# Optimization experiments

Hardware: AMD Instinct MI355X
Metric: run time of the kernel (lower is better)

The kernel has to match this reference:

```python
import jax, jax.numpy as jnp
import numpy as np
import math

HEAD = 4
HEAD_DIM = 16
K_ATT = 7
PAD_ATT = 3  # (dilation*(kernel_att-1)+1)//2 with dilation=1, kernel_att=7
K_CONV = 3


def closest_factor_to_sqrt(n):
    if n <= 1:
        return n
    sqrt_n = int(math.sqrt(n))
    if sqrt_n * sqrt_n == n:
        return sqrt_n
    best, best_diff = 1, float('inf')
    for i in range(sqrt_n, 0, -1):
        if n % i == 0:
            diff = abs(i - n // i)
            if diff < best_diff:
                best_diff, best = diff, i
    return best


def setup_inputs() -> dict:
    key = jax.random.key(0)
    ks = jax.random.split(key, 10)
    Cin, Cout = 64, 64
    x = jax.random.normal(ks[0], (2, Cin, 8, 32, 32), dtype=jnp.float32)
    w1 = jax.random.normal(ks[1], (Cout, Cin), dtype=jnp.float32) * 0.05
    b1 = jax.random.normal(ks[2], (Cout,), dtype=jnp.float32) * 0.01
    w2 = jax.random.normal(ks[3], (Cout, Cin), dtype=jnp.float32) * 0.05
    b2 = jax.random.normal(ks[4], (Cout,), dtype=jnp.float32) * 0.01
    w3 = jax.random.normal(ks[5], (Cout, Cin), dtype=jnp.float32) * 0.05
    b3 = jax.random.normal(ks[6], (Cout,), dtype=jnp.float32) * 0.01
    wp = jax.random.normal(ks[7], (HEAD_DIM, 3), dtype=jnp.float32) * 0.05
    bp = jnp.zeros((HEAD_DIM,), dtype=jnp.float32)
    wfc = jax.random.normal(ks[8], (K_CONV * K_CONV, 3 * HEAD), dtype=jnp.float32) * 0.05
    # dep_conv init per reset_parameters(): identity shift kernels, zero bias
    ident = jnp.eye(K_CONV * K_CONV, dtype=jnp.float32).reshape(K_CONV * K_CONV, K_CONV, K_CONV)
    wdep = jnp.tile(ident[None], (Cout, 1, 1, 1))  # (Cout, 9, 3, 3), groups=head_dim
    bdep = jnp.zeros((Cout,), dtype=jnp.float32)
    rate1 = jnp.array(0.5, dtype=jnp.float32)
    rate2 = jnp.array(0.5, dtype=jnp.float32)
    return {'x': x, 'w1': w1, 'b1': b1, 'w2': w2, 'b2': b2, 'w3': w3, 'b3': b3,
            'wp': wp, 'bp': bp, 'wfc': wfc, 'wdep': wdep, 'bdep': bdep,
            'rate1': rate1, 'rate2': rate2}


def _forward(x, w1, b1, w2, b2, w3, b3, wp, bp, wfc, wdep, bdep, rate1, rate2):
    conv1x1 = lambda t, wm, bias: jnp.einsum('oc,bcdwh->bodwh', wm, t) + bias[None, :, None, None, None]
    q = conv1x1(x, w1, b1)
    k = conv1x1(x, w2, b2)
    v = conv1x1(x, w3, b3)
    b, C, d, w, h = q.shape
    scaling = HEAD_DIM ** -0.5
    fh = closest_factor_to_sqrt(d)
    fw = d // fh
    H2, W2 = fh * h, fw * w  # flat reshape of (d, w, h) -> (H2, W2)

    # position encoding, torch position(d, h, w) -> (1, 3, d, w, h)
    loc_d = jnp.broadcast_to(jnp.linspace(-1.0, 1.0, d)[:, None, None], (d, w, h))
    loc_w = jnp.broadcast_to(jnp.linspace(-1.0, 1.0, w)[None, :, None], (d, w, h))
    loc_h = jnp.broadcast_to(jnp.linspace(-1.0, 1.0, h)[None, None, :], (d, w, h))
    loc = jnp.stack([loc_d, loc_w, loc_h], 0)[None].astype(x.dtype)
    pe = (jnp.einsum('oc,bcdwh->bodwh', wp, loc) + bp[None, :, None, None, None])
    pe = pe.reshape(1, HEAD_DIM, H2, W2)

    q_att = (q * scaling).reshape(b * HEAD, HEAD_DIM, H2, W2)
    k_att = k.reshape(b * HEAD, HEAD_DIM, H2, W2)
    v_att = v.reshape(b * HEAD, HEAD_DIM, H2, W2)

    def unfold(t):
        # nn.Unfold(kernel=7, stride=1) after ReflectionPad2d(3): (N, C, 49, H2, W2)
        p = jnp.pad(t, ((0, 0), (0, 0), (PAD_ATT, PAD_ATT), (PAD_ATT, PAD_ATT)), mode='reflect')
        return jnp.stack([p[:, :, i:i + H2, j:j + W2]
                          for i in range(K_ATT) for j in range(K_ATT)], axis=2)

    unfold_k = unfold(k_att)            # (b*head, hd, 49, H2, W2)
    unfold_rpe = unfold(pe)             # (1, hd, 49, H2, W2)
    scores = unfold_k + pe[:, :, None] - unfold_rpe
    att = jnp.einsum('nchw,nckhw->nkhw', q_att, scores)  # sum over head_dim
    att = jax.nn.softmax(att, axis=1)   # softmax over 49 window positions
    out_att = jnp.einsum('nkhw,nckhw->nchw', att, unfold(v_att))
    out_att = out_att.reshape(b, C, d, w, h)

    # conv-mixing branch
    L = d * w * h
    qkv = jnp.concatenate([q.reshape(b, HEAD, HEAD_DIM, L),
                           k.reshape(b, HEAD, HEAD_DIM, L),
                           v.reshape(b, HEAD, HEAD_DIM, L)], axis=1)  # (b, 3*head, hd, L)
    # fc: 1x1x1 conv over the 3*head channel axis (torch applies it unbatched after permute)
    f_all = jnp.einsum('oc,bcml->boml', wfc, qkv)         # (b, 9, hd, L)
    f_conv = f_all.reshape(b, K_CONV * K_CONV * HEAD_DIM, d, h * w)
    out_conv = jax.lax.conv_general_dilated(
        f_conv, wdep, window_strides=(1, 1), padding=[(1, 1), (1, 1)],
        dimension_numbers=('NCHW', 'OIHW', 'NCHW'), feature_group_count=HEAD_DIM)
    out_conv = out_conv + bdep[None, :, None, None]
    out_conv = out_conv.reshape(b, C, d, w, h)

    return rate1 * out_att + rate2 * out_conv


def reference(x, w1, b1, w2, b2, w3, b3, wp, bp, wfc, wdep, bdep, rate1, rate2):
    return _forward(x, w1, b1, w2, b2, w3, b3, wp, bp, wfc, wdep, bdep, rate1, rate2)
```

## Files before the change

### kernel.cpp

```cpp
#include <hip/hip_runtime.h>


__global__ __launch_bounds__(512) void qkvf_kernel(
    const float* __restrict__ x,
    const float* __restrict__ w1, const float* __restrict__ b1,
    const float* __restrict__ w2, const float* __restrict__ b2,
    const float* __restrict__ w3, const float* __restrict__ b3,
    const float* __restrict__ wfc,
    float* __restrict__ q, float* __restrict__ k, float* __restrict__ v,
    float* __restrict__ f)
{
    __shared__ float xs[64][64];
    __shared__ float wlds[3][64][64];

    int bx    = blockIdx.x;
    int ltile = bx & 127;
    int b     = bx >> 7;
    int l0    = ltile * 64;

    {
        float4* wl = (float4*)wlds;
        for (int t = threadIdx.x; t < 3072; t += 512) {
            int m   = t >> 10;
            int idx = t & 1023;
            const float* src = (m == 0) ? w1 : (m == 1) ? w2 : w3;
            wl[t] = ((const float4*)src)[idx];
        }
    }
    const float4* xg = (const float4*)(x + (size_t)b * 64 * 8192);
    for (int t = threadIdx.x; t < 1024; t += 512) {
        int ci = t >> 4, col = t & 15;
        *((float4*)&xs[ci][col * 4]) = xg[ci * 2048 + (l0 >> 2) + col];
    }
    __syncthreads();

    int lane = threadIdx.x & 63;
    int wv   = __builtin_amdgcn_readfirstlane(threadIdx.x >> 6);
    int l    = l0 + lane;
    int hd0  = 2 * wv;

    float qa[4][2], ka[4][2], va[4][2];
#pragma unroll
    for (int hh = 0; hh < 4; ++hh)
#pragma unroll
        for (int p = 0; p < 2; ++p) {
            int c = hh * 16 + hd0 + p;
            qa[hh][p] = b1[c]; ka[hh][p] = b2[c]; va[hh][p] = b3[c];
        }

#pragma unroll 4
    for (int c4 = 0; c4 < 16; ++c4) {
        float xv[4];
#pragma unroll
        for (int u = 0; u < 4; ++u) xv[u] = xs[c4 * 4 + u][lane];
#pragma unroll
        for (int hh = 0; hh < 4; ++hh)
#pragma unroll
            for (int p = 0; p < 2; ++p) {
                int c = hh * 16 + hd0 + p;
                float4 wq = *(const float4*)&wlds[0][c][c4 * 4];
                float4 wk = *(const float4*)&wlds[1][c][c4 * 4];
                float4 wx = *(const float4*)&wlds[2][c][c4 * 4];
                qa[hh][p] = fmaf(wq.x, xv[0], qa[hh][p]);
                qa[hh][p] = fmaf(wq.y, xv[1], qa[hh][p]);
                qa[hh][p] = fmaf(wq.z, xv[2], qa[hh][p]);
                qa[hh][p] = fmaf(wq.w, xv[3], qa[hh][p]);
                ka[hh][p] = fmaf(wk.x, xv[0], ka[hh][p]);
                ka[hh][p] = fmaf(wk.y, xv[1], ka[hh][p]);
                ka[hh][p] = fmaf(wk.z, xv[2], ka[hh][p]);
                ka[hh][p] = fmaf(wk.w, xv[3], ka[hh][p]);
                va[hh][p] = fmaf(wx.x, xv[0], va[hh][p]);
                va[hh][p] = fmaf(wx.y, xv[1], va[hh][p]);
                va[hh][p] = fmaf(wx.z, xv[2], va[hh][p]);
                va[hh][p] = fmaf(wx.w, xv[3], va[hh][p]);
            }
    }

#pragma unroll
    for (int hh = 0; hh < 4; ++hh)
#pragma unroll
        for (int p = 0; p < 2; ++p) {
            int c = hh * 16 + hd0 + p;
            size_t o = (size_t)(b * 64 + c) * 8192 + l;
            q[o] = qa[hh][p] * 0.25f;
            k[o] = ka[hh][p]; v[o] = va[hh][p];
        }

#pragma unroll
    for (int m = 0; m < 9; ++m)
#pragma unroll
        for (int p = 0; p < 2; ++p) {
            float acc = 0.f;
#pragma unroll
            for (int hh = 0; hh < 4; ++hh) {
                acc = fmaf(wfc[m * 12 + 0 + hh], qa[hh][p], acc);
                acc = fmaf(wfc[m * 12 + 4 + hh], ka[hh][p], acc);
                acc = fmaf(wfc[m * 12 + 8 + hh], va[hh][p], acc);
            }
            int hd = hd0 + p;
            f[((size_t)(b * 9 + m) * 16 + hd) * 8192 + l] = acc;
        }
}

__global__ __launch_bounds__(512, 4) void att_kernel(
    const float* __restrict__ q, const float* __restrict__ k,
    const float* __restrict__ v,
    const float* __restrict__ wp, const float* __restrict__ bp,
    const float* __restrict__ rate1p, float* __restrict__ out)
{
    __shared__ float kp[22 * 22 * 20];
    __shared__ float vt[22 * 22 * 20];

    int bx = blockIdx.x;
    int xt = bx & 7;
    int yt = (bx >> 3) & 3;
    int n  = bx >> 5;
    int head = n & 3;
    int b    = n >> 2;
    int y0 = yt * 16, x0 = xt * 16;

    const int NELEM = 16 * 22 * 22;
    for (int e = threadIdx.x; e < NELEM; e += 512) {
        int tx  = e % 22;
        int rem = e / 22;
        int ty  = rem % 22;
        int c   = rem / 22;
        int sy = y0 + ty - 3; if (sy < 0) sy = -sy; else if (sy >= 64)  sy = 126 - sy;
        int sx = x0 + tx - 3; if (sx < 0) sx = -sx; else if (sx >= 128) sx = 254 - sx;
        int l = sy * 128 + sx;
        size_t o = (size_t)(b * 64 + head * 16 + c) * 8192 + l;
        int dd = l >> 10, r2 = l & 1023, ww = r2 >> 5, hh = r2 & 31;
        float ld = dd * (2.0f / 7.0f)  - 1.0f;
        float lw = ww * (2.0f / 31.0f) - 1.0f;
        float lh = hh * (2.0f / 31.0f) - 1.0f;
        float pe = bp[c];
        pe = fmaf(wp[c * 3 + 0], ld, pe);
        pe = fmaf(wp[c * 3 + 1], lw, pe);
        pe = fmaf(wp[c * 3 + 2], lh, pe);
        int li = (ty * 22 + tx) * 20 + c;
        kp[li] = k[o] - pe;
        vt[li] = v[o];
    }
    __syncthreads();

    int pix  = threadIdx.x >> 1;
    int part = threadIdx.x & 1;
    int tx = pix & 15, ty = pix >> 4;
    int l = (y0 + ty) * 128 + (x0 + tx);
    int cb = part * 8;

    float qc[8];
#pragma unroll
    for (int c = 0; c < 8; ++c)
        qc[c] = q[(size_t)(b * 64 + head * 16 + cb + c) * 8192 + l];

    float lg[49];
#pragma unroll
    for (int i = 0; i < 7; ++i)
#pragma unroll
        for (int j = 0; j < 7; ++j) {
            const float4* p =
                (const float4*)&kp[((ty + i) * 22 + tx + j) * 20 + cb];
            float4 a = p[0], b4 = p[1];
            float acc =      qc[0] * a.x;
            acc = fmaf(qc[1], a.y,  acc); acc = fmaf(qc[2], a.z,  acc);
            acc = fmaf(qc[3], a.w,  acc); acc = fmaf(qc[4], b4.x, acc);
            acc = fmaf(qc[5], b4.y, acc); acc = fmaf(qc[6], b4.z, acc);
            acc = fmaf(qc[7], b4.w, acc);
            lg[i * 7 + j] = acc;
        }
#pragma unroll
    for (int kk = 0; kk < 49; ++kk)
        lg[kk] += __shfl_xor(lg[kk], 1, 64);

    float mx = lg[0];
#pragma unroll
    for (int kk = 1; kk < 49; ++kk) mx = fmaxf(mx, lg[kk]);
    float se = 0.f;
#pragma unroll
    for (int kk = 0; kk < 49; ++kk) { lg[kk] = __expf(lg[kk] - mx); se += lg[kk]; }
    float scale = rate1p[0] / se;

    float oc[8];
#pragma unroll
    for (int c = 0; c < 8; ++c) oc[c] = 0.f;
#pragma unroll
    for (int i = 0; i < 7; ++i)
#pragma unroll
        for (int j = 0; j < 7; ++j) {
            float wgt = lg[i * 7 + j];
            const float4* p =
                (const float4*)&vt[((ty + i) * 22 + tx + j) * 20 + cb];
            float4 a = p[0], b4 = p[1];
            oc[0] = fmaf(wgt, a.x,  oc[0]); oc[1] = fmaf(wgt, a.y,  oc[1]);
            oc[2] = fmaf(wgt, a.z,  oc[2]); oc[3] = fmaf(wgt, a.w,  oc[3]);
            oc[4] = fmaf(wgt, b4.x, oc[4]); oc[5] = fmaf(wgt, b4.y, oc[5]);
            oc[6] = fmaf(wgt, b4.z, oc[6]); oc[7] = fmaf(wgt, b4.w, oc[7]);
        }

#pragma unroll
    for (int c = 0; c < 8; ++c)
        out[(size_t)(b * 64 + head * 16 + cb + c) * 8192 + l] = oc[c] * scale;
}

__global__ __launch_bounds__(256) void conv_kernel(
    const float* __restrict__ f,
    const float* __restrict__ wdep, const float* __restrict__ bdep,
    const float* __restrict__ rate2p, float* __restrict__ out)
{
    __shared__ float ft[9][8][66];

    int bx = blockIdx.x;
    int xt = bx & 15;
    int g  = (bx >> 4) & 15;
    int b  = bx >> 8;
    int x0 = xt * 64;

    const int NE = 9 * 8 * 66;
    for (int e = threadIdx.x; e < NE; e += 256) {
        int xx  = e % 66;
        int rem = e / 66;
        int y = rem % 8, i = rem / 8;
        int gx = x0 + xx - 1;
        float val = 0.f;
        if (gx >= 0 && gx < 1024) {
            int c144 = g * 9 + i;
            val = f[((size_t)(b * 144 + c144)) * 8192 + y * 1024 + gx];
        }
        ft[i][y][xx] = val;
    }
    __syncthreads();

    int xl = threadIdx.x & 63;
    int op = __builtin_amdgcn_readfirstlane(threadIdx.x >> 6);
    int o  = g * 4 + op;
    float rate2 = rate2p[0];

    float acc[8];
#pragma unroll
    for (int y = 0; y < 8; ++y) acc[y] = 0.f;

    for (int i = 0; i < 9; ++i) {
        float fr[10][3];
#pragma unroll
        for (int dx = 0; dx < 3; ++dx) { fr[0][dx] = 0.f; fr[9][dx] = 0.f; }
#pragma unroll
        for (int y = 0; y < 8; ++y)
#pragma unroll
            for (int dx = 0; dx < 3; ++dx)
                fr[y + 1][dx] = ft[i][y][xl + dx];
#pragma unroll
        for (int ky = 0; ky < 3; ++ky)
#pragma unroll
            for (int kx = 0; kx < 3; ++kx) {
                float wvv = wdep[((o * 9 + i) * 3 + ky) * 3 + kx];
#pragma unroll
                for (int y = 0; y < 8; ++y)
                    acc[y] = fmaf(wvv, fr[y + ky][kx], acc[y]);
            }
    }

    float bd = bdep[o];
#pragma unroll
    for (int y = 0; y < 8; ++y) {
        size_t idx = (size_t)(b * 64 + o) * 8192 + y * 1024 + x0 + xl;
        out[idx] = out[idx] + rate2 * (acc[y] + bd);
    }
}

extern "C" void kernel_launch(void* const* d_in, const int* in_sizes, int n_in,
                              void* d_out, int out_size, void* d_ws, size_t ws_size,
                              hipStream_t stream)
{
    (void)in_sizes; (void)n_in; (void)out_size; (void)ws_size;
    const float* x     = (const float*)d_in[0];
    const float* w1    = (const float*)d_in[1];
    const float* b1    = (const float*)d_in[2];
    const float* w2    = (const float*)d_in[3];
    const float* b2    = (const float*)d_in[4];
    const float* w3    = (const float*)d_in[5];
    const float* b3    = (const float*)d_in[6];
    const float* wp    = (const float*)d_in[7];
    const float* bp    = (const float*)d_in[8];
    const float* wfc   = (const float*)d_in[9];
    const float* wdep  = (const float*)d_in[10];
    const float* bdep  = (const float*)d_in[11];
    const float* rate1 = (const float*)d_in[12];
    const float* rate2 = (const float*)d_in[13];
    float* out = (float*)d_out;

    float* wsf = (float*)d_ws;
    float* q = wsf;
    float* k = wsf + 1048576;
    float* v = wsf + 2097152;
    float* f = wsf + 3145728;

    qkvf_kernel<<<256, 512, 0, stream>>>(x, w1, b1, w2, b2, w3, b3, wfc,
                                         q, k, v, f);
    att_kernel <<<256, 512, 0, stream>>>(q, k, v, wp, bp, rate1, out);
    conv_kernel<<<512, 256, 0, stream>>>(f, wdep, bdep, rate2, out);
}
```

Measured before the change: 127.1 us.

## Retile qkv projection: each thread computes two spatial positions for one head-dim

The projection kernel now splits output channels across two block halves (8 head-dims each) and gives each thread two adjacent spatial positions instead of two channels at one position. Each weight float4 read from shared memory now feeds two FMAs, and all global stores become float2. This lowers shared-memory traffic per FMA and widens stores, but x tiles are loaded twice (once per half) and the x tile in LDS grows.

```diff
diff --git a/kernel.cpp b/kernel.cpp
--- a/kernel.cpp
+++ b/kernel.cpp
@@ -10,96 +10,112 @@
     float* __restrict__ q, float* __restrict__ k, float* __restrict__ v,
     float* __restrict__ f)
 {
-    __shared__ float xs[64][64];
-    __shared__ float wlds[3][64][64];
+    __shared__ float xs[64][128];
+    __shared__ float wlds[3][32][64];
 
     int bx    = blockIdx.x;
-    int ltile = bx & 127;
+    int ltile = bx & 63;
+    int half  = (bx >> 6) & 1;
     int b     = bx >> 7;
-    int l0    = ltile * 64;
-
-    {
-        float4* wl = (float4*)wlds;
-        for (int t = threadIdx.x; t < 3072; t += 512) {
-            int m   = t >> 10;
-            int idx = t & 1023;
-            const float* src = (m == 0) ? w1 : (m == 1) ? w2 : w3;
-            wl[t] = ((const float4*)src)[idx];
-        }
+    int l0    = ltile * 128;
+    int hdb   = half * 8;
+
+    for (int t = threadIdx.x; t < 1536; t += 512) {
+        int mat = t >> 9;
+        int r   = t & 511;
+        int cl  = r >> 4;
+        int col = r & 15;
+        int hh = cl >> 3, hdl = cl & 7;
+        int c  = hh * 16 + hdb + hdl;
+        const float* src = (mat == 0) ? w1 : (mat == 1) ? w2 : w3;
+        ((float4*)wlds)[t] = ((const float4*)src)[c * 16 + col];
     }
     const float4* xg = (const float4*)(x + (size_t)b * 64 * 8192);
-    for (int t = threadIdx.x; t < 1024; t += 512) {
-        int ci = t >> 4, col = t & 15;
-        *((float4*)&xs[ci][col * 4]) = xg[ci * 2048 + (l0 >> 2) + col];
+    for (int t = threadIdx.x; t < 2048; t += 512) {
+        int ci = t >> 5, col = t & 31;
+        ((float4*)xs)[t] = xg[ci * 2048 + (l0 >> 2) + col];
     }
     __syncthreads();
 
     int lane = threadIdx.x & 63;
     int wv   = __builtin_amdgcn_readfirstlane(threadIdx.x >> 6);
-    int l    = l0 + lane;
-    int hd0  = 2 * wv;
+    int hd   = hdb + wv;
+    int ll   = 2 * lane;
 
     float qa[4][2], ka[4][2], va[4][2];
 #pragma unroll
-    for (int hh = 0; hh < 4; ++hh)
-#pragma unroll
-        for (int p = 0; p < 2; ++p) {
-            int c = hh * 16 + hd0 + p;
-            qa[hh][p] = b1[c]; ka[hh][p] = b2[c]; va[hh][p] = b3[c];
-        }
+    for (int hh = 0; hh < 4; ++hh) {
+        int c = hh * 16 + hd;
+        qa[hh][0] = qa[hh][1] = b1[c];
+        ka[hh][0] = ka[hh][1] = b2[c];
+        va[hh][0] = va[hh][1] = b3[c];
+    }
 
 #pragma unroll 4
     for (int c4 = 0; c4 < 16; ++c4) {
-        float xv[4];
-#pragma unroll
-        for (int u = 0; u < 4; ++u) xv[u] = xs[c4 * 4 + u][lane];
-#pragma unroll
-        for (int hh = 0; hh < 4; ++hh)
-#pragma unroll
-            for (int p = 0; p < 2; ++p) {
-                int c = hh * 16 + hd0 + p;
-                float4 wq = *(const float4*)&wlds[0][c][c4 * 4];
-                float4 wk = *(const float4*)&wlds[1][c][c4 * 4];
-                float4 wx = *(const float4*)&wlds[2][c][c4 * 4];
-                qa[hh][p] = fmaf(wq.x, xv[0], qa[hh][p]);
-                qa[hh][p] = fmaf(wq.y, xv[1], qa[hh][p]);
-                qa[hh][p] = fmaf(wq.z, xv[2], qa[hh][p]);
-                qa[hh][p] = fmaf(wq.w, xv[3], qa[hh][p]);
-                ka[hh][p] = fmaf(wk.x, xv[0], ka[hh][p]);
-                ka[hh][p] = fmaf(wk.y, xv[1], ka[hh][p]);
-                ka[hh][p] = fmaf(wk.z, xv[2], ka[hh][p]);
-                ka[hh][p] = fmaf(wk.w, xv[3], ka[hh][p]);
-                va[hh][p] = fmaf(wx.x, xv[0], va[hh][p]);
-                va[hh][p] = fmaf(wx.y, xv[1], va[hh][p]);
-                va[hh][p] = fmaf(wx.z, xv[2], va[hh][p]);
-                va[hh][p] = fmaf(wx.w, xv[3], va[hh][p]);
-            }
-    }
-
-#pragma unroll
-    for (int hh = 0; hh < 4; ++hh)
-#pragma unroll
-        for (int p = 0; p < 2; ++p) {
-            int c = hh * 16 + hd0 + p;
-            size_t o = (size_t)(b * 64 + c) * 8192 + l;
-            q[o] = qa[hh][p] * 0.25f;
-            k[o] = ka[hh][p]; v[o] = va[hh][p];
-        }
-
-#pragma unroll
-    for (int m = 0; m < 9; ++m)
-#pragma unroll
-        for (int p = 0; p < 2; ++p) {
-            float acc = 0.f;
-#pragma unroll
-            for (int hh = 0; hh < 4; ++hh) {
-                acc = fmaf(wfc[m * 12 + 0 + hh], qa[hh][p], acc);
-                acc = fmaf(wfc[m * 12 + 4 + hh], ka[hh][p], acc);
-                acc = fmaf(wfc[m * 12 + 8 + hh], va[hh][p], acc);
-            }
-            int hd = hd0 + p;
-            f[((size_t)(b * 9 + m) * 16 + hd) * 8192 + l] = acc;
-        }
+        float2 xv[4];
+#pragma unroll
+        for (int u = 0; u < 4; ++u)
+            xv[u] = *(const float2*)&xs[c4 * 4 + u][ll];
+#pragma unroll
+        for (int hh = 0; hh < 4; ++hh) {
+            int cl = hh * 8 + wv;
+            float4 wq = *(const float4*)&wlds[0][cl][c4 * 4];
+            float4 wk = *(const float4*)&wlds[1][cl][c4 * 4];
+            float4 wx = *(const float4*)&wlds[2][cl][c4 * 4];
+            qa[hh][0] = fmaf(wq.x, xv[0].x, qa[hh][0]);
+            qa[hh][1] = fmaf(wq.x, xv[0].y, qa[hh][1]);
+            qa[hh][0] = fmaf(wq.y, xv[1].x, qa[hh][0]);
+            qa[hh][1] = fmaf(wq.y, xv[1].y, qa[hh][1]);
+            qa[hh][0] = fmaf(wq.z, xv[2].x, qa[hh][0]);
+            qa[hh][1] = fmaf(wq.z, xv[2].y, qa[hh][1]);
+            qa[hh][0] = fmaf(wq.w, xv[3].x, qa[hh][0]);
+            qa[hh][1] = fmaf(wq.w, xv[3].y, qa[hh][1]);
+
+            ka[hh][0] = fmaf(wk.x, xv[0].x, ka[hh][0]);
+            ka[hh][1] = fmaf(wk.x, xv[0].y, ka[hh][1]);
+            ka[hh][0] = fmaf(wk.y, xv[1].x, ka[hh][0]);
+            ka[hh][1] = fmaf(wk.y, xv[1].y, ka[hh][1]);
+            ka[hh][0] = fmaf(wk.z, xv[2].x, ka[hh][0]);
+            ka[hh][1] = fmaf(wk.z, xv[2].y, ka[hh][1]);
+            ka[hh][0] = fmaf(wk.w, xv[3].x, ka[hh][0]);
+            ka[hh][1] = fmaf(wk.w, xv[3].y, ka[hh][1]);
+
+            va[hh][0] = fmaf(wx.x, xv[0].x, va[hh][0]);
+            va[hh][1] = fmaf(wx.x, xv[0].y, va[hh][1]);
+            va[hh][0] = fmaf(wx.y, xv[1].x, va[hh][0]);
+            va[hh][1] = fmaf(wx.y, xv[1].y, va[hh][1]);
+            va[hh][0] = fmaf(wx.z, xv[2].x, va[hh][0]);
+            va[hh][1] = fmaf(wx.z, xv[2].y, va[hh][1]);
+            va[hh][0] = fmaf(wx.w, xv[3].x, va[hh][0]);
+            va[hh][1] = fmaf(wx.w, xv[3].y, va[hh][1]);
+        }
+    }
+
+#pragma unroll
+    for (int hh = 0; hh < 4; ++hh) {
+        int c = hh * 16 + hd;
+        size_t o = (size_t)(b * 64 + c) * 8192 + l0 + ll;
+        *(float2*)&q[o] = make_float2(qa[hh][0] * 0.25f, qa[hh][1] * 0.25f);
+        *(float2*)&k[o] = make_float2(ka[hh][0], ka[hh][1]);
+        *(float2*)&v[o] = make_float2(va[hh][0], va[hh][1]);
+    }
+
+#pragma unroll
+    for (int m = 0; m < 9; ++m) {
+        float a0 = 0.f, a1 = 0.f;
+#pragma unroll
+        for (int hh = 0; hh < 4; ++hh) {
+            a0 = fmaf(wfc[m * 12 + 0 + hh], qa[hh][0], a0);
+            a1 = fmaf(wfc[m * 12 + 0 + hh], qa[hh][1], a1);
+            a0 = fmaf(wfc[m * 12 + 4 + hh], ka[hh][0], a0);
+            a1 = fmaf(wfc[m * 12 + 4 + hh], ka[hh][1], a1);
+            a0 = fmaf(wfc[m * 12 + 8 + hh], va[hh][0], a0);
+            a1 = fmaf(wfc[m * 12 + 8 + hh], va[hh][1], a1);
+        }
+        size_t o = ((size_t)(b * 9 + m) * 16 + hd) * 8192 + l0 + ll;
+        *(float2*)&f[o] = make_float2(a0, a1);
+    }
 }
 
 __global__ __launch_bounds__(512, 4) void att_kernel(
```

Result: faster. 120.2 us (-5.5%).
